# Optimization experiments

Measured on AMD Instinct MI355X. Metric: run time of the kernel, lower is better.

## Reference

```python
import jax, jax.numpy as jnp
import numpy as np

N = 8192        # number of nodes (adjacency is N x N)
F_IN = 256      # in_features
F_OUT = 256     # out_features


def setup_inputs() -> dict:
    key = jax.random.key(0)
    k_x, k_adj, k_kernel, k_bias, k_beta = jax.random.split(key, 5)
    x = jax.random.normal(k_x, (N, F_IN), dtype=jnp.float32)
    adj = jax.random.uniform(k_adj, (N, N), dtype=jnp.float32)  # dense non-negative adjacency buffer
    # xavier-uniform-like scale for the kernel
    limit = float(np.sqrt(6.0 / (F_IN + F_OUT)))
    kernel = jax.random.uniform(k_kernel, (F_IN, F_OUT), dtype=jnp.float32, minval=-limit, maxval=limit)
    bias = 0.01 * jax.random.normal(k_bias, (F_OUT,), dtype=jnp.float32)
    beta = 0.01 * jax.random.normal(k_beta, (N,), dtype=jnp.float32)
    return {"x": x, "adj": adj, "kernel": kernel, "bias": bias, "beta": beta}


def reference(x, adj, kernel, bias, beta):
    # Original: diag(1/(rowsum(adj)+beta)) @ (adj + diag(beta)) @ x @ kernel + bias
    # Fused form: row-scale and diagonal-add applied without materializing NxN diag matrices.
    scale = jnp.reciprocal(jnp.sum(adj, axis=1) + beta)          # [N]
    agg = adj @ x + beta[:, None] * x                             # (adj + diag(beta)) @ x  -> [N, F_IN]
    return (scale[:, None] * agg) @ kernel + bias                 # [N, F_OUT]
```

## Files before the change

### kernel.cpp

```cpp
#include <hip/hip_runtime.h>
#include <hip/hip_bf16.h>


typedef __attribute__((ext_vector_type(8))) short  short8;
typedef __attribute__((ext_vector_type(4))) short  short4v;
typedef __attribute__((ext_vector_type(4))) float  floatx4;

#define N_NODES 8192
#define F_DIM   256

#define ASYNC16(g, l)                                                          \
  __builtin_amdgcn_global_load_lds(                                           \
      (const __attribute__((address_space(1))) void*)(g),                     \
      (__attribute__((address_space(3))) void*)(l), 16, 0, 0)

__device__ __forceinline__ unsigned short f2bf(float f) {
  unsigned u = __float_as_uint(f);
  return (unsigned short)((u + 0x7FFFu + ((u >> 16) & 1u)) >> 16);
}

__device__ __forceinline__ short8 pack_bf16x8(floatx4 a, floatx4 b) {
  short8 r;
  r[0] = (short)f2bf(a.x); r[1] = (short)f2bf(a.y);
  r[2] = (short)f2bf(a.z); r[3] = (short)f2bf(a.w);
  r[4] = (short)f2bf(b.x); r[5] = (short)f2bf(b.y);
  r[6] = (short)f2bf(b.z); r[7] = (short)f2bf(b.w);
  return r;
}

__global__ __launch_bounds__(256) void tile_bf16_kernel(
    const float* __restrict__ src, unsigned short* __restrict__ dst, int K) {
  const int Nn = F_DIM;
  int cid = blockIdx.x * 256 + threadIdx.x;
  int per_kblk = Nn * 4;
  int kblk = cid / per_kblk;
  int rem  = cid - kblk * per_kblk;
  int n16 = rem >> 6;
  int kg  = (rem >> 4) & 3;
  int nl  = rem & 15;
  int n = n16 * 16 + nl;
  int k = kblk * 32 + kg * 8;
  const float* s = src + (size_t)k * Nn + n;
  floatx4 v0, v1;
  v0.x = s[0];
  v0.y = s[(size_t)Nn];
  v0.z = s[(size_t)2 * Nn];
  v0.w = s[(size_t)3 * Nn];
  v1.x = s[(size_t)4 * Nn];
  v1.y = s[(size_t)5 * Nn];
  v1.z = s[(size_t)6 * Nn];
  v1.w = s[(size_t)7 * Nn];
  *(short8*)(dst + (size_t)cid * 8) = pack_bf16x8(v0, v1);
}

template <int KS>
__global__ __launch_bounds__(256, 3) void stage1_kernel(
    const float* __restrict__ adj, const unsigned short* __restrict__ xbt,
    float* __restrict__ part, float* __restrict__ rsp) {
  __shared__ float          At[2][64 * 32];
  __shared__ unsigned short Bt[64 * F_DIM];

  const int tid = threadIdx.x;
  const int w  = tid >> 6;
  const int l  = tid & 63;
  const int kq = l >> 4;
  const int ml = l & 15;
  const int m0 = blockIdx.x * 64;
  const int ks = blockIdx.y;
  const int kbeg   = ks * (N_NODES / KS);
  const int KSTEPS = (N_NODES / KS) / 64;

  const int arow = w * 16 + (l >> 3);
  const int srcg = (l & 7) ^ ((l >> 3) & 7);
  const float* agp0 = adj + (size_t)(m0 + arow) * N_NODES + kbeg + srcg * 4;
  const float* agp1 = agp0 + (size_t)8 * N_NODES;
  float* a0d0 = At[0] + (w * 2) * 256;
  float* a0d1 = At[0] + (w * 2 + 1) * 256;
  float* a1d0 = At[1] + (w * 2) * 256;
  float* a1d1 = At[1] + (w * 2 + 1) * 256;
  const unsigned short* bgp =
      xbt + (size_t)(kbeg / 32) * (32 * F_DIM) + w * 4096 + l * 8;
  unsigned short* bldst = Bt + w * 4096;

  int aoff0[4], aoff1[4];
#pragma unroll
  for (int mf = 0; mf < 4; ++mf) {
    int m = mf * 16 + ml;
    aoff0[mf] = m * 32 + (((kq * 2)     ^ (m & 7)) * 4);
    aoff1[mf] = m * 32 + (((kq * 2 + 1) ^ (m & 7)) * 4);
  }

  floatx4 acc[4][4];
  const floatx4 zf4 = {0.f, 0.f, 0.f, 0.f};
#pragma unroll
  for (int mf = 0; mf < 4; ++mf)
#pragma unroll
    for (int nf = 0; nf < 4; ++nf) acc[mf][nf] = zf4;
  float rsum[4] = {0.f, 0.f, 0.f, 0.f};

  for (int s = 0; s < KSTEPS; ++s) {
    ASYNC16(agp0,      a0d0);
    ASYNC16(agp1,      a0d1);
    ASYNC16(agp0 + 32, a1d0);
    ASYNC16(agp1 + 32, a1d1);
#pragma unroll
    for (int i = 0; i < 8; ++i) ASYNC16(bgp + i * 512, bldst + i * 512);
    agp0 += 64; agp1 += 64; bgp += 64 * F_DIM;
    __syncthreads();

#pragma unroll
    for (int h = 0; h < 2; ++h) {
      short8 af[4];
#pragma unroll
      for (int mf = 0; mf < 4; ++mf) {
        floatx4 a0 = *(const floatx4*)(At[h] + aoff0[mf]);
        floatx4 a1 = *(const floatx4*)(At[h] + aoff1[mf]);
        if (w == 0)
          rsum[mf] += (a0.x + a0.y + a0.z + a0.w) + (a1.x + a1.y + a1.z + a1.w);
        af[mf] = pack_bf16x8(a0, a1);
      }
#pragma unroll
      for (int nf = 0; nf < 4; ++nf) {
        short8 bv = *(const short8*)(Bt + h * 8192 + (w * 4 + nf) * 512 +
                                     kq * 128 + ml * 8);
#pragma unroll
        for (int mf = 0; mf < 4; ++mf)
          acc[mf][nf] = __builtin_amdgcn_mfma_f32_16x16x32_bf16(
              af[mf], bv, acc[mf][nf], 0, 0, 0);
      }
    }
    __syncthreads();
  }

  float* pout = part + (size_t)ks * N_NODES * F_DIM;
#pragma unroll
  for (int mf = 0; mf < 4; ++mf)
#pragma unroll
    for (int nf = 0; nf < 4; ++nf) {
      int col = w * 64 + nf * 16 + ml;
#pragma unroll
      for (int r = 0; r < 4; ++r) {
        int row = m0 + mf * 16 + kq * 4 + r;
        pout[(size_t)row * F_DIM + col] = acc[mf][nf][r];
      }
    }

  if (w == 0) {
#pragma unroll
    for (int mf = 0; mf < 4; ++mf) {
      float v = rsum[mf];
      v += __shfl_xor(v, 16);
      v += __shfl_xor(v, 32);
      if (kq == 0) rsp[ks * N_NODES + m0 + mf * 16 + ml] = v;
    }
  }
}

template <int KS>
__global__ __launch_bounds__(256, 2) void stage2_kernel(
    const float* part, const float* __restrict__ rsp,
    const float* __restrict__ x, const float* __restrict__ beta,
    const float* __restrict__ bias, const unsigned short* __restrict__ wbt,
    float* out) {
  __shared__ unsigned short At[32 * 32];
  __shared__ unsigned short Bt[32 * F_DIM];
  __shared__ float sscale[32];
  __shared__ float sbeta[32];

  const int tid = threadIdx.x;
  const int w  = tid >> 6;
  const int l  = tid & 63;
  const int kq = l >> 4;
  const int ml = l & 15;
  const int m0 = blockIdx.x * 32;
  const int ar = tid >> 3;
  const int ag = tid & 7;

  if (tid < 32) {
    float rs = 0.f;
#pragma unroll
    for (int p = 0; p < KS; ++p) rs += rsp[p * N_NODES + m0 + tid];
    float b = beta[m0 + tid];
    sbeta[tid]  = b;
    sscale[tid] = 1.0f / (rs + b);
  }
  __syncthreads();

  floatx4 acc[2][4];
  const floatx4 zf4 = {0.f, 0.f, 0.f, 0.f};
#pragma unroll
  for (int mf = 0; mf < 2; ++mf)
#pragma unroll
    for (int nf = 0; nf < 4; ++nf) acc[mf][nf] = zf4;

  const unsigned short* bgp = wbt + (w * 4) * 512 + l * 8;
  unsigned short* bldst = Bt + (w * 4) * 512;
  const float bb = sbeta[ar];
  const float sc = sscale[ar];
  unsigned short* adst = At + ar * 32 + (((ag >> 1) ^ (ar & 3)) * 8) + (ag & 1) * 4;

  for (int s = 0; s < 8; ++s) {
    ASYNC16(bgp,        bldst);
    ASYNC16(bgp +  512, bldst +  512);
    ASYNC16(bgp + 1024, bldst + 1024);
    ASYNC16(bgp + 1536, bldst + 1536);
    bgp += 32 * F_DIM;

    {
      size_t off = (size_t)(m0 + ar) * F_DIM + s * 32 + ag * 4;
      floatx4 v = *(const floatx4*)(x + off) * bb;
#pragma unroll
      for (int p = 0; p < KS; ++p)
        v += *(const floatx4*)(part + (size_t)p * N_NODES * F_DIM + off);
      v *= sc;
      short4v pv;
      pv[0] = (short)f2bf(v.x); pv[1] = (short)f2bf(v.y);
      pv[2] = (short)f2bf(v.z); pv[3] = (short)f2bf(v.w);
      *(short4v*)adst = pv;
    }
    __syncthreads();

    short8 af[2];
#pragma unroll
    for (int mf = 0; mf < 2; ++mf) {
      int m = mf * 16 + ml;
      af[mf] = *(const short8*)(At + m * 32 + ((kq ^ (m & 3)) * 8));
    }
#pragma unroll
    for (int nf = 0; nf < 4; ++nf) {
      short8 bv = *(const short8*)(Bt + (w * 4 + nf) * 512 + kq * 128 + ml * 8);
#pragma unroll
      for (int mf = 0; mf < 2; ++mf)
        acc[mf][nf] =
            __builtin_amdgcn_mfma_f32_16x16x32_bf16(af[mf], bv, acc[mf][nf], 0, 0, 0);
    }
    __syncthreads();
  }

#pragma unroll
  for (int nf = 0; nf < 4; ++nf) {
    int col = w * 64 + nf * 16 + ml;
    float bv = bias[col];
#pragma unroll
    for (int mf = 0; mf < 2; ++mf)
#pragma unroll
      for (int r = 0; r < 4; ++r) {
        int row = m0 + mf * 16 + kq * 4 + r;
        out[(size_t)row * F_DIM + col] = acc[mf][nf][r] + bv;
      }
  }
}

extern "C" void kernel_launch(void* const* d_in, const int* in_sizes, int n_in,
                              void* d_out, int out_size, void* d_ws, size_t ws_size,
                              hipStream_t stream) {
  const float* x    = (const float*)d_in[0];
  const float* adj  = (const float*)d_in[1];
  const float* kern = (const float*)d_in[2];
  const float* bias = (const float*)d_in[3];
  const float* beta = (const float*)d_in[4];
  float* out = (float*)d_out;

  char* ws = (char*)d_ws;
  unsigned short* xbt = (unsigned short*)ws;
  unsigned short* wbt = xbt + (size_t)N_NODES * F_DIM;
  float* rsp  = (float*)(wbt + F_DIM * F_DIM);
  float* part = (float*)((char*)rsp + 8 * N_NODES * sizeof(float));

  const size_t base    = (size_t)N_NODES * F_DIM * 2 + (size_t)F_DIM * F_DIM * 2 +
                         8 * (size_t)N_NODES * 4;
  const size_t part_sz = (size_t)N_NODES * F_DIM * 4;

  tile_bf16_kernel<<<(N_NODES * F_DIM / 8) / 256, 256, 0, stream>>>(x, xbt, N_NODES);
  tile_bf16_kernel<<<(F_DIM * F_DIM / 8) / 256, 256, 0, stream>>>(kern, wbt, F_DIM);

  if (ws_size >= base + 8 * part_sz) {
    stage1_kernel<8><<<dim3(128, 8), 256, 0, stream>>>(adj, xbt, part, rsp);
    stage2_kernel<8><<<256, 256, 0, stream>>>(part, rsp, x, beta, bias, wbt, out);
  } else if (ws_size >= base + 4 * part_sz) {
    stage1_kernel<4><<<dim3(128, 4), 256, 0, stream>>>(adj, xbt, part, rsp);
    stage2_kernel<4><<<256, 256, 0, stream>>>(part, rsp, x, beta, bias, wbt, out);
  } else {
    stage1_kernel<1><<<dim3(128, 1), 256, 0, stream>>>(adj, xbt, out, rsp);
    stage2_kernel<1><<<256, 256, 0, stream>>>(out, rsp, x, beta, bias, wbt, out);
  }
}
```

Before: 457.7 us.

## Drop LDS staging and load operands straight into registers in both GEMM stages

Stage1 no longer stages the adjacency and x tiles through shared memory with async global-to-LDS copies and per-step barriers. Each wave now loads its own 32x32 adjacency fragment and a 128-column bf16 x slice directly into registers and issues MFMAs with no synchronisation. Stage2 is also rewritten without LDS: 16-row blocks build the bf16 A fragment in registers from x, the partials and the scale, and read the weight fragments straight from global, with twice as many blocks. The goal is to remove barrier stalls and LDS traffic, at the cost of duplicated global/L2 reads across waves and no explicit prefetch to hide latency.

```diff
diff --git a/kernel.cpp b/kernel.cpp
--- a/kernel.cpp
+++ b/kernel.cpp
@@ -3,16 +3,10 @@
 
 
 typedef __attribute__((ext_vector_type(8))) short  short8;
-typedef __attribute__((ext_vector_type(4))) short  short4v;
 typedef __attribute__((ext_vector_type(4))) float  floatx4;
 
 #define N_NODES 8192
 #define F_DIM   256
-
-#define ASYNC16(g, l)                                                          \
-  __builtin_amdgcn_global_load_lds(                                           \
-      (const __attribute__((address_space(1))) void*)(g),                     \
-      (__attribute__((address_space(3))) void*)(l), 16, 0, 0)
 
 __device__ __forceinline__ unsigned short f2bf(float f) {
   unsigned u = __float_as_uint(f);
@@ -57,197 +51,140 @@
 __global__ __launch_bounds__(256, 3) void stage1_kernel(
     const float* __restrict__ adj, const unsigned short* __restrict__ xbt,
     float* __restrict__ part, float* __restrict__ rsp) {
-  __shared__ float          At[2][64 * 32];
-  __shared__ unsigned short Bt[64 * F_DIM];
-
   const int tid = threadIdx.x;
-  const int w  = tid >> 6;
-  const int l  = tid & 63;
-  const int kq = l >> 4;
-  const int ml = l & 15;
-  const int m0 = blockIdx.x * 64;
-  const int ks = blockIdx.y;
-  const int kbeg   = ks * (N_NODES / KS);
-  const int KSTEPS = (N_NODES / KS) / 64;
-
-  const int arow = w * 16 + (l >> 3);
-  const int srcg = (l & 7) ^ ((l >> 3) & 7);
-  const float* agp0 = adj + (size_t)(m0 + arow) * N_NODES + kbeg + srcg * 4;
-  const float* agp1 = agp0 + (size_t)8 * N_NODES;
-  float* a0d0 = At[0] + (w * 2) * 256;
-  float* a0d1 = At[0] + (w * 2 + 1) * 256;
-  float* a1d0 = At[1] + (w * 2) * 256;
-  float* a1d1 = At[1] + (w * 2 + 1) * 256;
-  const unsigned short* bgp =
-      xbt + (size_t)(kbeg / 32) * (32 * F_DIM) + w * 4096 + l * 8;
-  unsigned short* bldst = Bt + w * 4096;
-
-  int aoff0[4], aoff1[4];
-#pragma unroll
-  for (int mf = 0; mf < 4; ++mf) {
-    int m = mf * 16 + ml;
-    aoff0[mf] = m * 32 + (((kq * 2)     ^ (m & 7)) * 4);
-    aoff1[mf] = m * 32 + (((kq * 2 + 1) ^ (m & 7)) * 4);
-  }
-
-  floatx4 acc[4][4];
+  const int w   = tid >> 6;
+  const int h   = w >> 1;
+  const int c   = w & 1;
+  const int l   = tid & 63;
+  const int kq  = l >> 4;
+  const int ml  = l & 15;
+  const int m0  = blockIdx.x * 64;
+  const int ks  = blockIdx.y;
+  const int kbeg  = ks * (N_NODES / KS);
+  const int STEPS = (N_NODES / KS) / 32;
+
+  const float* abase = adj + (size_t)(m0 + h * 32 + ml) * N_NODES + kbeg + kq * 8;
+  const unsigned short* bbase =
+      xbt + (size_t)(kbeg / 32) * (32 * F_DIM) + (c * 8) * 512 + kq * 128 + ml * 8;
+
+  floatx4 acc[2][8];
   const floatx4 zf4 = {0.f, 0.f, 0.f, 0.f};
 #pragma unroll
-  for (int mf = 0; mf < 4; ++mf)
-#pragma unroll
-    for (int nf = 0; nf < 4; ++nf) acc[mf][nf] = zf4;
-  float rsum[4] = {0.f, 0.f, 0.f, 0.f};
-
-  for (int s = 0; s < KSTEPS; ++s) {
-    ASYNC16(agp0,      a0d0);
-    ASYNC16(agp1,      a0d1);
-    ASYNC16(agp0 + 32, a1d0);
-    ASYNC16(agp1 + 32, a1d1);
-#pragma unroll
-    for (int i = 0; i < 8; ++i) ASYNC16(bgp + i * 512, bldst + i * 512);
-    agp0 += 64; agp1 += 64; bgp += 64 * F_DIM;
-    __syncthreads();
-
-#pragma unroll
-    for (int h = 0; h < 2; ++h) {
-      short8 af[4];
-#pragma unroll
-      for (int mf = 0; mf < 4; ++mf) {
-        floatx4 a0 = *(const floatx4*)(At[h] + aoff0[mf]);
-        floatx4 a1 = *(const floatx4*)(At[h] + aoff1[mf]);
-        if (w == 0)
-          rsum[mf] += (a0.x + a0.y + a0.z + a0.w) + (a1.x + a1.y + a1.z + a1.w);
-        af[mf] = pack_bf16x8(a0, a1);
-      }
-#pragma unroll
-      for (int nf = 0; nf < 4; ++nf) {
-        short8 bv = *(const short8*)(Bt + h * 8192 + (w * 4 + nf) * 512 +
-                                     kq * 128 + ml * 8);
-#pragma unroll
-        for (int mf = 0; mf < 4; ++mf)
-          acc[mf][nf] = __builtin_amdgcn_mfma_f32_16x16x32_bf16(
-              af[mf], bv, acc[mf][nf], 0, 0, 0);
-      }
-    }
-    __syncthreads();
+  for (int mf = 0; mf < 2; ++mf)
+#pragma unroll
+    for (int nf = 0; nf < 8; ++nf) acc[mf][nf] = zf4;
+  float rsum[2] = {0.f, 0.f};
+
+  for (int s = 0; s < STEPS; ++s) {
+    floatx4 a0[2], a1[2];
+#pragma unroll
+    for (int mf = 0; mf < 2; ++mf) {
+      const float* p = abase + (size_t)mf * 16 * N_NODES + s * 32;
+      a0[mf] = *(const floatx4*)p;
+      a1[mf] = *(const floatx4*)(p + 4);
+    }
+    short8 bv[8];
+#pragma unroll
+    for (int nf = 0; nf < 8; ++nf)
+      bv[nf] = *(const short8*)(bbase + (size_t)s * (32 * F_DIM) + nf * 512);
+
+    short8 af[2];
+#pragma unroll
+    for (int mf = 0; mf < 2; ++mf) {
+      if (c == 0)
+        rsum[mf] += (a0[mf].x + a0[mf].y + a0[mf].z + a0[mf].w) +
+                    (a1[mf].x + a1[mf].y + a1[mf].z + a1[mf].w);
+      af[mf] = pack_bf16x8(a0[mf], a1[mf]);
+    }
+#pragma unroll
+    for (int nf = 0; nf < 8; ++nf)
+#pragma unroll
+      for (int mf = 0; mf < 2; ++mf)
+        acc[mf][nf] = __builtin_amdgcn_mfma_f32_16x16x32_bf16(
+            af[mf], bv[nf], acc[mf][nf], 0, 0, 0);
   }
 
   float* pout = part + (size_t)ks * N_NODES * F_DIM;
 #pragma unroll
-  for (int mf = 0; mf < 4; ++mf)
-#pragma unroll
-    for (int nf = 0; nf < 4; ++nf) {
-      int col = w * 64 + nf * 16 + ml;
+  for (int mf = 0; mf < 2; ++mf)
+#pragma unroll
+    for (int nf = 0; nf < 8; ++nf) {
+      int col = c * 128 + nf * 16 + ml;
 #pragma unroll
       for (int r = 0; r < 4; ++r) {
-        int row = m0 + mf * 16 + kq * 4 + r;
+        int row = m0 + h * 32 + mf * 16 + kq * 4 + r;
         pout[(size_t)row * F_DIM + col] = acc[mf][nf][r];
       }
     }
 
-  if (w == 0) {
-#pragma unroll
-    for (int mf = 0; mf < 4; ++mf) {
+  if (c == 0) {
+#pragma unroll
+    for (int mf = 0; mf < 2; ++mf) {
       float v = rsum[mf];
       v += __shfl_xor(v, 16);
       v += __shfl_xor(v, 32);
-      if (kq == 0) rsp[ks * N_NODES + m0 + mf * 16 + ml] = v;
+      if (kq == 0) rsp[ks * N_NODES + m0 + h * 32 + mf * 16 + ml] = v;
     }
   }
 }
 
 template <int KS>
-__global__ __launch_bounds__(256, 2) void stage2_kernel(
+__global__ __launch_bounds__(256, 3) void stage2_kernel(
     const float* part, const float* __restrict__ rsp,
     const float* __restrict__ x, const float* __restrict__ beta,
     const float* __restrict__ bias, const unsigned short* __restrict__ wbt,
     float* out) {
-  __shared__ unsigned short At[32 * 32];
-  __shared__ unsigned short Bt[32 * F_DIM];
-  __shared__ float sscale[32];
-  __shared__ float sbeta[32];
-
   const int tid = threadIdx.x;
-  const int w  = tid >> 6;
-  const int l  = tid & 63;
-  const int kq = l >> 4;
-  const int ml = l & 15;
-  const int m0 = blockIdx.x * 32;
-  const int ar = tid >> 3;
-  const int ag = tid & 7;
-
-  if (tid < 32) {
-    float rs = 0.f;
-#pragma unroll
-    for (int p = 0; p < KS; ++p) rs += rsp[p * N_NODES + m0 + tid];
-    float b = beta[m0 + tid];
-    sbeta[tid]  = b;
-    sscale[tid] = 1.0f / (rs + b);
-  }
+  const int w   = tid >> 6;
+  const int l   = tid & 63;
+  const int kq  = l >> 4;
+  const int ml  = l & 15;
+  const int m0  = blockIdx.x * 16;
+  const int row = m0 + ml;
+
+  float bb = beta[row];
+  float rs = 0.f;
+#pragma unroll
+  for (int p = 0; p < KS; ++p) rs += rsp[p * N_NODES + row];
+  const float sc = 1.0f / (rs + bb);
+
+  floatx4 acc[4];
+  const floatx4 zf4 = {0.f, 0.f, 0.f, 0.f};
+#pragma unroll
+  for (int nf = 0; nf < 4; ++nf) acc[nf] = zf4;
+
+  const size_t rowoff = (size_t)row * F_DIM + kq * 8;
+
+  for (int s = 0; s < 8; ++s) {
+    size_t off = rowoff + s * 32;
+    floatx4 v0 = *(const floatx4*)(x + off);
+    floatx4 v1 = *(const floatx4*)(x + off + 4);
+    v0 *= bb; v1 *= bb;
+#pragma unroll
+    for (int p = 0; p < KS; ++p) {
+      const float* pp = part + (size_t)p * N_NODES * F_DIM + off;
+      v0 += *(const floatx4*)pp;
+      v1 += *(const floatx4*)(pp + 4);
+    }
+    v0 *= sc; v1 *= sc;
+    short8 af = pack_bf16x8(v0, v1);
+#pragma unroll
+    for (int nf = 0; nf < 4; ++nf) {
+      short8 bv = *(const short8*)(wbt + (size_t)s * (32 * F_DIM) +
+                                   (w * 4 + nf) * 512 + kq * 128 + ml * 8);
+      acc[nf] = __builtin_amdgcn_mfma_f32_16x16x32_bf16(af, bv, acc[nf], 0, 0, 0);
+    }
+  }
+
   __syncthreads();
-
-  floatx4 acc[2][4];
-  const floatx4 zf4 = {0.f, 0.f, 0.f, 0.f};
-#pragma unroll
-  for (int mf = 0; mf < 2; ++mf)
-#pragma unroll
-    for (int nf = 0; nf < 4; ++nf) acc[mf][nf] = zf4;
-
-  const unsigned short* bgp = wbt + (w * 4) * 512 + l * 8;
-  unsigned short* bldst = Bt + (w * 4) * 512;
-  const float bb = sbeta[ar];
-  const float sc = sscale[ar];
-  unsigned short* adst = At + ar * 32 + (((ag >> 1) ^ (ar & 3)) * 8) + (ag & 1) * 4;
-
-  for (int s = 0; s < 8; ++s) {
-    ASYNC16(bgp,        bldst);
-    ASYNC16(bgp +  512, bldst +  512);
-    ASYNC16(bgp + 1024, bldst + 1024);
-    ASYNC16(bgp + 1536, bldst + 1536);
-    bgp += 32 * F_DIM;
-
-    {
-      size_t off = (size_t)(m0 + ar) * F_DIM + s * 32 + ag * 4;
-      floatx4 v = *(const floatx4*)(x + off) * bb;
-#pragma unroll
-      for (int p = 0; p < KS; ++p)
-        v += *(const floatx4*)(part + (size_t)p * N_NODES * F_DIM + off);
-      v *= sc;
-      short4v pv;
-      pv[0] = (short)f2bf(v.x); pv[1] = (short)f2bf(v.y);
-      pv[2] = (short)f2bf(v.z); pv[3] = (short)f2bf(v.w);
-      *(short4v*)adst = pv;
-    }
-    __syncthreads();
-
-    short8 af[2];
-#pragma unroll
-    for (int mf = 0; mf < 2; ++mf) {
-      int m = mf * 16 + ml;
-      af[mf] = *(const short8*)(At + m * 32 + ((kq ^ (m & 3)) * 8));
-    }
-#pragma unroll
-    for (int nf = 0; nf < 4; ++nf) {
-      short8 bv = *(const short8*)(Bt + (w * 4 + nf) * 512 + kq * 128 + ml * 8);
-#pragma unroll
-      for (int mf = 0; mf < 2; ++mf)
-        acc[mf][nf] =
-            __builtin_amdgcn_mfma_f32_16x16x32_bf16(af[mf], bv, acc[mf][nf], 0, 0, 0);
-    }
-    __syncthreads();
-  }
 
 #pragma unroll
   for (int nf = 0; nf < 4; ++nf) {
     int col = w * 64 + nf * 16 + ml;
-    float bv = bias[col];
-#pragma unroll
-    for (int mf = 0; mf < 2; ++mf)
-#pragma unroll
-      for (int r = 0; r < 4; ++r) {
-        int row = m0 + mf * 16 + kq * 4 + r;
-        out[(size_t)row * F_DIM + col] = acc[mf][nf][r] + bv;
-      }
+    float bvs = bias[col];
+#pragma unroll
+    for (int r = 0; r < 4; ++r)
+      out[(size_t)(m0 + kq * 4 + r) * F_DIM + col] = acc[nf][r] + bvs;
   }
 }
 
@@ -276,12 +213,12 @@
 
   if (ws_size >= base + 8 * part_sz) {
     stage1_kernel<8><<<dim3(128, 8), 256, 0, stream>>>(adj, xbt, part, rsp);
-    stage2_kernel<8><<<256, 256, 0, stream>>>(part, rsp, x, beta, bias, wbt, out);
+    stage2_kernel<8><<<512, 256, 0, stream>>>(part, rsp, x, beta, bias, wbt, out);
   } else if (ws_size >= base + 4 * part_sz) {
     stage1_kernel<4><<<dim3(128, 4), 256, 0, stream>>>(adj, xbt, part, rsp);
-    stage2_kernel<4><<<256, 256, 0, stream>>>(part, rsp, x, beta, bias, wbt, out);
+    stage2_kernel<4><<<512, 256, 0, stream>>>(part, rsp, x, beta, bias, wbt, out);
   } else {
     stage1_kernel<1><<<dim3(128, 1), 256, 0, stream>>>(adj, xbt, out, rsp);
-    stage2_kernel<1><<<256, 256, 0, stream>>>(out, rsp, x, beta, bias, wbt, out);
-  }
-}
+    stage2_kernel<1><<<512, 256, 0, stream>>>(out, rsp, x, beta, bias, wbt, out);
+  }
+}
```

After: 493.6 us. +7.8%, slower.
